# Kernel optimization log

Hardware: AMD Instinct MI355X
Metric: run time of the kernel (lower is better)

Reference implementation:

```python
import jax, jax.numpy as jnp
import numpy as np

ENCODER_DIM = 2048
DECODER_DIM = 512
ATTENTION_DIM = 512
BATCH = 512
NUM_PIXELS = 196


def setup_inputs() -> dict:
    key = jax.random.key(0)
    k = jax.random.split(key, 8)
    s_e = 1.0 / np.sqrt(ENCODER_DIM)
    s_d = 1.0 / np.sqrt(DECODER_DIM)
    s_a = 1.0 / np.sqrt(ATTENTION_DIM)
    return {
        "encoder_out": jax.random.normal(k[0], (BATCH, NUM_PIXELS, ENCODER_DIM), jnp.float32),
        "decoder_hidden": jax.random.normal(k[1], (BATCH, DECODER_DIM), jnp.float32),
        "W_enc": jax.random.uniform(k[2], (ENCODER_DIM, ATTENTION_DIM), jnp.float32, -s_e, s_e),
        "b_enc": jax.random.uniform(k[3], (ATTENTION_DIM,), jnp.float32, -s_e, s_e),
        "W_dec": jax.random.uniform(k[4], (DECODER_DIM, ATTENTION_DIM), jnp.float32, -s_d, s_d),
        "b_dec": jax.random.uniform(k[5], (ATTENTION_DIM,), jnp.float32, -s_d, s_d),
        "W_full": jax.random.uniform(k[6], (ATTENTION_DIM,), jnp.float32, -s_a, s_a),
        "b_full": jax.random.uniform(k[7], (), jnp.float32, -s_a, s_a),
    }


def reference(encoder_out, decoder_hidden, W_enc, b_enc, W_dec, b_dec, W_full, b_full):
    # att1: [B, P, A], att2: [B, A]
    att1 = jnp.einsum('bpe,ea->bpa', encoder_out, W_enc) + b_enc
    att2 = decoder_hidden @ W_dec + b_dec
    # scores: [B, P]
    scores = jnp.einsum('bpa,a->bp', jnp.tanh(att1 + att2[:, None, :]), W_full) + b_full
    alpha = jax.nn.softmax(scores, axis=1)
    context = jnp.einsum('bpe,bp->be', encoder_out, alpha)
    return context, alpha
```

## Files before the change

kernel.cpp:

```cpp
#include <hip/hip_runtime.h>
#include <hip/hip_bf16.h>
#include <stdint.h>

#define BATCH 512
#define PIX   196
#define EDIM  2048
#define DDIM  512
#define ADIM  512
#define MROWS (BATCH*PIX)

#define BM 256
#define BN 256
#define BK 64
#define NT (EDIM/BK)

typedef __attribute__((ext_vector_type(8))) short bf16x8;
typedef __attribute__((ext_vector_type(8))) float f32x8;
typedef __attribute__((ext_vector_type(8))) __bf16 bf16v8;
typedef __attribute__((ext_vector_type(4))) float f32x4;

#define GLL16(g, lptr) __builtin_amdgcn_global_load_lds( \
    (const __attribute__((address_space(1))) void*)(g),  \
    (__attribute__((address_space(3))) void*)(lptr), 16, 0, 0)

static __device__ __forceinline__ unsigned short f2bf(float f) {
  union { float f; uint32_t u; } v; v.f = f;
  uint32_t u = v.u;
  return (unsigned short)((u + 0x7FFFu + ((u >> 16) & 1u)) >> 16);
}

static __device__ __forceinline__ bf16x8 cvt8(float4 a, float4 b) {
  f32x8 v = {a.x, a.y, a.z, a.w, b.x, b.y, b.z, b.w};
  bf16v8 c = __builtin_convertvector(v, bf16v8);
  bf16x8 r;
  __builtin_memcpy(&r, &c, 16);
  return r;
}

__global__ void k_transpose_wenc(const float* __restrict__ W,
                                 unsigned short* __restrict__ Bt) {
  __shared__ float tile[32][33];
  const int kt = blockIdx.x;
  const int nt = blockIdx.y;
  const int tx = threadIdx.x, ty = threadIdx.y;
#pragma unroll
  for (int j = 0; j < 4; j++)
    tile[ty + 8*j][tx] = W[(size_t)(kt*32 + ty + 8*j)*ADIM + nt*32 + tx];
  __syncthreads();
#pragma unroll
  for (int j = 0; j < 4; j++)
    Bt[(size_t)(nt*32 + ty + 8*j)*EDIM + kt*32 + tx] = f2bf(tile[tx][ty + 8*j]);
}

__global__ void k_att2(const float* __restrict__ H, const float* __restrict__ Wd,
                       const float* __restrict__ bd, float* __restrict__ att2) {
  __shared__ float h[DDIM];
  const int b = blockIdx.x;
  const int t = threadIdx.x;
  h[t]       = H[(size_t)b*DDIM + t];
  h[t + 256] = H[(size_t)b*DDIM + t + 256];
  __syncthreads();
  float a0 = 0.f, a1 = 0.f;
#pragma unroll 8
  for (int k = 0; k < DDIM; k++) {
    const float hv = h[k];
    a0 += hv * Wd[(size_t)k*ADIM + t];
    a1 += hv * Wd[(size_t)k*ADIM + t + 256];
  }
  att2[(size_t)b*ADIM + t]       = a0 + bd[t];
  att2[(size_t)b*ADIM + t + 256] = a1 + bd[t + 256];
}

__global__ __launch_bounds__(512) void k_gemm_scores(
    const float* __restrict__ enc,
    const unsigned short* __restrict__ Bt,
    const float* __restrict__ b_enc,
    const float* __restrict__ att2,
    const float* __restrict__ W_full,
    float* __restrict__ scores)
{
  __shared__ __align__(16) char ldsA[2*32768];
  __shared__ __align__(16) char ldsB[2*32768];
  __shared__ float sc[BM];

  const int t   = threadIdx.x;
  const int l   = t & 63;
  const int wid = t >> 6;
  const int wr  = wid >> 2;
  const int wc  = wid & 3;

  const int orig = blockIdx.x;
  const int tile = (orig & 7) * 98 + (orig >> 3);
  const int bm0 = (tile >> 1) * BM;
  const int bn0 = (tile & 1) * BN;

  if (t < BM) sc[t] = 0.f;

  const int arow = t >> 1;
  const int ah   = t & 1;
  const float* srcA = enc + (size_t)(bm0 + arow) * EDIM + ah * 32;
  int wA[4];
#pragma unroll
  for (int j = 0; j < 4; j++)
    wA[j] = arow*128 + (((ah*4 + j) ^ (arow & 7)) * 16);

  const unsigned short* srcB[4];
#pragma unroll
  for (int j = 0; j < 4; j++) {
    const int row = (t >> 3) + j*64;
    srcB[j] = Bt + (size_t)(bn0 + row) * EDIM + ((t & 7) ^ (row & 7)) * 8;
  }
  const int dstB = wid * 1024;

  const int l15 = l & 15, hi = l >> 4;
  const int sw  = l15 & 7;
  const int c0  = (hi ^ sw) * 16;
  const int c1  = ((4 + hi) ^ sw) * 16;
  const int baseA = (wr*128 + l15) * 128;
  const int baseB = (wc*64  + l15) * 128;

  float4 ar[8];
  bf16x8 af[4], bfr[4];
  f32x4 acc[8][4] = {};

#define A_ISSUE(KT) do {                                         \
    const float* _s = srcA + (size_t)(KT) * BK;                  \
    _Pragma("unroll")                                            \
    for (int j = 0; j < 8; j++) ar[j] = ((const float4*)_s)[j];  \
  } while (0)

#define B_GLLJ(NXT, KT, J) \
    GLL16(srcB[J] + (size_t)(KT) * BK, ldsB + (NXT)*32768 + dstB + (J)*8192)

#define A_WRITE(NXT) do {                                        \
    _Pragma("unroll")                                            \
    for (int j = 0; j < 4; j++) {                                \
      bf16x8 w = cvt8(ar[2*j], ar[2*j + 1]);                     \
      *(bf16x8*)(ldsA + (NXT)*32768 + wA[j]) = w;                \
    }                                                            \
  } while (0)

#define DSREAD_B(CUR, CKS) do {                                  \
    _Pragma("unroll")                                            \
    for (int ni = 0; ni < 4; ni++)                               \
      bfr[ni] = *(const bf16x8*)(ldsB + (CUR)*32768 + baseB + ni*2048 + (CKS)); \
  } while (0)

#define DSREAD_A(CUR, CKS, MOFF) do {                            \
    _Pragma("unroll")                                            \
    for (int mi = 0; mi < 4; mi++)                               \
      af[mi] = *(const bf16x8*)(ldsA + (CUR)*32768 + baseA + (mi+(MOFF))*2048 + (CKS)); \
  } while (0)

#define BARLG()                                                  \
    __builtin_amdgcn_s_barrier();                                \
    asm volatile("s_waitcnt lgkmcnt(0)" ::: "memory");           \
    __builtin_amdgcn_sched_barrier(0);                           \
    __builtin_amdgcn_s_setprio(1)

#define ENDBAR()                                                 \
    __builtin_amdgcn_s_setprio(0);                               \
    __builtin_amdgcn_s_barrier()

#define MF16(MOFF) do {                                          \
    _Pragma("unroll")                                            \
    for (int mi = 0; mi < 4; mi++)                               \
      _Pragma("unroll")                                          \
      for (int ni = 0; ni < 4; ni++)                             \
        acc[mi+(MOFF)][ni] = __builtin_amdgcn_mfma_f32_16x16x32_bf16( \
            af[mi], bfr[ni], acc[mi+(MOFF)][ni], 0, 0, 0);       \
  } while (0)

#define TILE(KT, CUR, NXT) do {                                  \
                                                         \
    A_ISSUE((KT)+1);                                             \
    DSREAD_B(CUR, c0); DSREAD_A(CUR, c0, 0);                     \
    BARLG(); MF16(0); ENDBAR();                                  \
                                                         \
    B_GLLJ(NXT, (KT)+1, 0); B_GLLJ(NXT, (KT)+1, 1);              \
    DSREAD_A(CUR, c0, 4);                                        \
    BARLG(); MF16(4); ENDBAR();                                  \
                                                         \
    B_GLLJ(NXT, (KT)+1, 2); B_GLLJ(NXT, (KT)+1, 3);              \
    DSREAD_B(CUR, c1); DSREAD_A(CUR, c1, 0);                     \
    BARLG(); MF16(0); ENDBAR();                                  \
                                                         \
    asm volatile("s_waitcnt vmcnt(4)" ::: "memory");             \
    A_WRITE(NXT);                                                \
    DSREAD_A(CUR, c1, 4);                                        \
    BARLG(); MF16(4);                                            \
    asm volatile("s_waitcnt vmcnt(0)" ::: "memory");             \
    ENDBAR();                                                    \
  } while (0)

  A_ISSUE(0);
  B_GLLJ(0, 0, 0); B_GLLJ(0, 0, 1); B_GLLJ(0, 0, 2); B_GLLJ(0, 0, 3);
  asm volatile("s_waitcnt vmcnt(4)" ::: "memory");
  A_WRITE(0);
  asm volatile("s_waitcnt vmcnt(0) lgkmcnt(0)" ::: "memory");
  __builtin_amdgcn_s_barrier();

  for (int kb = 0; kb < 30; kb += 2) {
    TILE(kb,     0, 1);
    TILE(kb + 1, 1, 0);
  }
  TILE(30, 0, 1);

#pragma unroll
  for (int ks = 0; ks < 2; ks++) {
    const int cks = ks ? c1 : c0;
    DSREAD_B(1, cks);
    DSREAD_A(1, cks, 0);
    MF16(0);
    DSREAD_A(1, cks, 4);
    MF16(4);
  }

  float be[4], wf[4];
  int colv[4];
#pragma unroll
  for (int ni = 0; ni < 4; ni++) {
    colv[ni] = bn0 + wc*64 + ni*16 + l15;
    be[ni] = b_enc[colv[ni]];
    wf[ni] = W_full[colv[ni]];
  }
#pragma unroll
  for (int mi = 0; mi < 8; mi++) {
#pragma unroll
    for (int e = 0; e < 4; e++) {
      const int row_l = wr*128 + mi*16 + hi*4 + e;
      const unsigned gr = (unsigned)(bm0 + row_l);
      const unsigned b  = gr / 196u;
      float s = 0.f;
#pragma unroll
      for (int ni = 0; ni < 4; ni++) {
        const float v = acc[mi][ni][e] + be[ni] + att2[(size_t)b*ADIM + colv[ni]];
        s += tanhf(v) * wf[ni];
      }
      s += __shfl_xor(s, 1); s += __shfl_xor(s, 2);
      s += __shfl_xor(s, 4); s += __shfl_xor(s, 8);
      if (l15 == 0) atomicAdd(&sc[row_l], s);
    }
  }
  __syncthreads();
  if (t < BM) atomicAdd(&scores[bm0 + t], sc[t]);
}

__global__ void k_softmax(float* __restrict__ sa) {
  __shared__ float red[256];
  const int b = blockIdx.x, t = threadIdx.x;
  const float v = (t < PIX) ? sa[(size_t)b*PIX + t] : -1e30f;
  red[t] = v; __syncthreads();
  for (int s2 = 128; s2 > 0; s2 >>= 1) {
    if (t < s2) red[t] = fmaxf(red[t], red[t + s2]);
    __syncthreads();
  }
  const float m = red[0]; __syncthreads();
  const float e = (t < PIX) ? __expf(v - m) : 0.f;
  red[t] = e; __syncthreads();
  for (int s2 = 128; s2 > 0; s2 >>= 1) {
    if (t < s2) red[t] += red[t + s2];
    __syncthreads();
  }
  const float inv = 1.f / red[0];
  if (t < PIX) sa[(size_t)b*PIX + t] = e * inv;
}

__global__ __launch_bounds__(512) void k_context(
    const float* __restrict__ enc, const float* __restrict__ alpha,
    float* __restrict__ ctx) {
  __shared__ float al[PIX];
  const int b = blockIdx.x, t = threadIdx.x;
  if (t < PIX) al[t] = alpha[(size_t)b*PIX + t];
  __syncthreads();
  const float4* e4 = (const float4*)(enc + (size_t)b * PIX * EDIM);
  float4 acc = {0.f, 0.f, 0.f, 0.f};
#pragma unroll 4
  for (int p = 0; p < PIX; p++) {
    const float4 v = e4[(size_t)p * (EDIM/4) + t];
    const float a = al[p];
    acc.x += v.x * a; acc.y += v.y * a; acc.z += v.z * a; acc.w += v.w * a;
  }
  ((float4*)(ctx + (size_t)b * EDIM))[t] = acc;
}

extern "C" void kernel_launch(void* const* d_in, const int* in_sizes, int n_in,
                              void* d_out, int out_size, void* d_ws, size_t ws_size,
                              hipStream_t stream) {
  (void)in_sizes; (void)n_in; (void)out_size; (void)ws_size;
  const float* enc   = (const float*)d_in[0];
  const float* hid   = (const float*)d_in[1];
  const float* Wenc  = (const float*)d_in[2];
  const float* benc  = (const float*)d_in[3];
  const float* Wdec  = (const float*)d_in[4];
  const float* bdec  = (const float*)d_in[5];
  const float* Wfull = (const float*)d_in[6];

  unsigned short* Bt = (unsigned short*)d_ws;
  float* att2 = (float*)((char*)d_ws + (size_t)ADIM * EDIM * 2);
  float* ctx   = (float*)d_out;
  float* alpha = (float*)d_out + (size_t)BATCH * EDIM;

  hipMemsetAsync(alpha, 0, (size_t)MROWS * sizeof(float), stream);
  k_transpose_wenc<<<dim3(64, 16), dim3(32, 8), 0, stream>>>(Wenc, Bt);
  k_att2<<<BATCH, 256, 0, stream>>>(hid, Wdec, bdec, att2);
  k_gemm_scores<<<784, 512, 0, stream>>>(enc, Bt, benc, att2, Wfull, alpha);
  k_softmax<<<BATCH, 256, 0, stream>>>(alpha);
  k_context<<<BATCH, 512, 0, stream>>>(enc, alpha, ctx);
}
```

Before: 734.4 us.

## Stream fp32 A tiles directly to LDS with triple-buffered BK=32 pipeline

The fp32 encoder tile is now fetched with global_load_lds straight into LDS instead of through registers, and converted to bf16 when the MFMA fragments are read. The K-step shrinks from 64 to 32 and the loop uses three LDS buffers, prefetching two tiles ahead with partial vmcnt waits. This is meant to remove the register-staged load, convert and write path and deepen the load pipeline. In exchange, A LDS traffic doubles because it is stored as fp32, each wave repeats the fp32-to-bf16 conversion, and LDS use grows to about 144KB per block.

Result: faster. 667.3 us (-9.1%).

```diff
diff --git a/kernel.cpp b/kernel.cpp
--- a/kernel.cpp
+++ b/kernel.cpp
@@ -11,7 +11,7 @@
 
 #define BM 256
 #define BN 256
-#define BK 64
+#define BK 32
 #define NT (EDIM/BK)
 
 typedef __attribute__((ext_vector_type(8))) short bf16x8;
@@ -79,9 +79,10 @@
     const float* __restrict__ W_full,
     float* __restrict__ scores)
 {
-  __shared__ __align__(16) char ldsA[2*32768];
-  __shared__ __align__(16) char ldsB[2*32768];
+  __shared__ __align__(16) char ldsbuf[3*49152];
   __shared__ float sc[BM];
+  char* ldsA = ldsbuf;
+  char* ldsB = ldsbuf + 98304;
 
   const int t   = threadIdx.x;
   const int l   = t & 63;
@@ -96,60 +97,58 @@
 
   if (t < BM) sc[t] = 0.f;
 
-  const int arow = t >> 1;
-  const int ah   = t & 1;
-  const float* srcA = enc + (size_t)(bm0 + arow) * EDIM + ah * 32;
-  int wA[4];
-#pragma unroll
-  for (int j = 0; j < 4; j++)
-    wA[j] = arow*128 + (((ah*4 + j) ^ (arow & 7)) * 16);
-
-  const unsigned short* srcB[4];
+  const float* srcA[4];
 #pragma unroll
   for (int j = 0; j < 4; j++) {
-    const int row = (t >> 3) + j*64;
-    srcB[j] = Bt + (size_t)(bn0 + row) * EDIM + ((t & 7) ^ (row & 7)) * 8;
-  }
-  const int dstB = wid * 1024;
+    const int idx = j*512 + t;
+    const int row = idx >> 3, c = idx & 7;
+    srcA[j] = enc + (size_t)(bm0 + row) * EDIM + (c ^ (row & 7)) * 4;
+  }
+  const unsigned short* srcB[2];
+#pragma unroll
+  for (int j = 0; j < 2; j++) {
+    const int idx = j*512 + t;
+    const int row = idx >> 2, c = idx & 3;
+    srcB[j] = Bt + (size_t)(bn0 + row) * EDIM + (c ^ (row & 3)) * 8;
+  }
+  const int dstb = wid * 1024;
 
   const int l15 = l & 15, hi = l >> 4;
-  const int sw  = l15 & 7;
-  const int c0  = (hi ^ sw) * 16;
-  const int c1  = ((4 + hi) ^ sw) * 16;
-  const int baseA = (wr*128 + l15) * 128;
-  const int baseB = (wc*64  + l15) * 128;
-
-  float4 ar[8];
+  const int sw7 = l15 & 7, sw3 = l15 & 3;
+  const int addrA0 = (wr*128 + l15)*128 + (((2*hi)    ) ^ sw7)*16;
+  const int addrA1 = (wr*128 + l15)*128 + (((2*hi) + 1) ^ sw7)*16;
+  const int addrB  = (wc*64  + l15)*64  + (hi ^ sw3)*16;
+
   bf16x8 af[4], bfr[4];
   f32x4 acc[8][4] = {};
 
-#define A_ISSUE(KT) do {                                         \
-    const float* _s = srcA + (size_t)(KT) * BK;                  \
-    _Pragma("unroll")                                            \
-    for (int j = 0; j < 8; j++) ar[j] = ((const float4*)_s)[j];  \
-  } while (0)
-
-#define B_GLLJ(NXT, KT, J) \
-    GLL16(srcB[J] + (size_t)(KT) * BK, ldsB + (NXT)*32768 + dstB + (J)*8192)
-
-#define A_WRITE(NXT) do {                                        \
-    _Pragma("unroll")                                            \
-    for (int j = 0; j < 4; j++) {                                \
-      bf16x8 w = cvt8(ar[2*j], ar[2*j + 1]);                     \
-      *(bf16x8*)(ldsA + (NXT)*32768 + wA[j]) = w;                \
+#define A_GLL(WB, KT) do {                                       \
+    _Pragma("unroll")                                            \
+    for (int j = 0; j < 4; j++)                                  \
+      GLL16(srcA[j] + (size_t)(KT)*BK,                           \
+            ldsA + (WB)*32768 + j*8192 + dstb);                  \
+  } while (0)
+
+#define B_GLL(WB, KT) do {                                       \
+    _Pragma("unroll")                                            \
+    for (int j = 0; j < 2; j++)                                  \
+      GLL16(srcB[j] + (size_t)(KT)*BK,                           \
+            ldsB + (WB)*16384 + j*8192 + dstb);                  \
+  } while (0)
+
+#define DSREAD_A(BUF, MOFF) do {                                 \
+    _Pragma("unroll")                                            \
+    for (int mi = 0; mi < 4; mi++) {                             \
+      const float4 fa = *(const float4*)(ldsA + (BUF)*32768 + (mi+(MOFF))*2048 + addrA0); \
+      const float4 fb = *(const float4*)(ldsA + (BUF)*32768 + (mi+(MOFF))*2048 + addrA1); \
+      af[mi] = cvt8(fa, fb);                                     \
     }                                                            \
   } while (0)
 
-#define DSREAD_B(CUR, CKS) do {                                  \
+#define DSREAD_B(BUF) do {                                       \
     _Pragma("unroll")                                            \
     for (int ni = 0; ni < 4; ni++)                               \
-      bfr[ni] = *(const bf16x8*)(ldsB + (CUR)*32768 + baseB + ni*2048 + (CKS)); \
-  } while (0)
-
-#define DSREAD_A(CUR, CKS, MOFF) do {                            \
-    _Pragma("unroll")                                            \
-    for (int mi = 0; mi < 4; mi++)                               \
-      af[mi] = *(const bf16x8*)(ldsA + (CUR)*32768 + baseA + (mi+(MOFF))*2048 + (CKS)); \
+      bfr[ni] = *(const bf16x8*)(ldsB + (BUF)*16384 + ni*1024 + addrB); \
   } while (0)
 
 #define BARLG()                                                  \
@@ -171,50 +170,35 @@
             af[mi], bfr[ni], acc[mi+(MOFF)][ni], 0, 0, 0);       \
   } while (0)
 
-#define TILE(KT, CUR, NXT) do {                                  \
+#define TILE(T, BUF, WBUF, DO_STAGE, WVM) do {                   \
                                                          \
-    A_ISSUE((KT)+1);                                             \
-    DSREAD_B(CUR, c0); DSREAD_A(CUR, c0, 0);                     \
+    if (DO_STAGE) A_GLL(WBUF, (T)+2);                            \
+    DSREAD_B(BUF); DSREAD_A(BUF, 0);                             \
     BARLG(); MF16(0); ENDBAR();                                  \
                                                          \
-    B_GLLJ(NXT, (KT)+1, 0); B_GLLJ(NXT, (KT)+1, 1);              \
-    DSREAD_A(CUR, c0, 4);                                        \
-    BARLG(); MF16(4); ENDBAR();                                  \
-                                                         \
-    B_GLLJ(NXT, (KT)+1, 2); B_GLLJ(NXT, (KT)+1, 3);              \
-    DSREAD_B(CUR, c1); DSREAD_A(CUR, c1, 0);                     \
-    BARLG(); MF16(0); ENDBAR();                                  \
-                                                         \
-    asm volatile("s_waitcnt vmcnt(4)" ::: "memory");             \
-    A_WRITE(NXT);                                                \
-    DSREAD_A(CUR, c1, 4);                                        \
+    if (DO_STAGE) B_GLL(WBUF, (T)+2);                            \
+    DSREAD_A(BUF, 4);                                            \
     BARLG(); MF16(4);                                            \
-    asm volatile("s_waitcnt vmcnt(0)" ::: "memory");             \
+    if ((WVM) == 6)      asm volatile("s_waitcnt vmcnt(6)" ::: "memory"); \
+    else if ((WVM) == 0) asm volatile("s_waitcnt vmcnt(0)" ::: "memory"); \
     ENDBAR();                                                    \
   } while (0)
 
-  A_ISSUE(0);
-  B_GLLJ(0, 0, 0); B_GLLJ(0, 0, 1); B_GLLJ(0, 0, 2); B_GLLJ(0, 0, 3);
-  asm volatile("s_waitcnt vmcnt(4)" ::: "memory");
-  A_WRITE(0);
-  asm volatile("s_waitcnt vmcnt(0) lgkmcnt(0)" ::: "memory");
+  A_GLL(0, 0); B_GLL(0, 0);
+  A_GLL(1, 1); B_GLL(1, 1);
+  asm volatile("s_waitcnt vmcnt(6)" ::: "memory");
   __builtin_amdgcn_s_barrier();
 
-  for (int kb = 0; kb < 30; kb += 2) {
-    TILE(kb,     0, 1);
-    TILE(kb + 1, 1, 0);
-  }
-  TILE(30, 0, 1);
-
-#pragma unroll
-  for (int ks = 0; ks < 2; ks++) {
-    const int cks = ks ? c1 : c0;
-    DSREAD_B(1, cks);
-    DSREAD_A(1, cks, 0);
-    MF16(0);
-    DSREAD_A(1, cks, 4);
-    MF16(4);
-  }
+  for (int kb = 0; kb < 60; kb += 3) {
+    TILE(kb,     0, 2, true, 6);
+    TILE(kb + 1, 1, 0, true, 6);
+    TILE(kb + 2, 2, 1, true, 6);
+  }
+  TILE(60, 0, 2, true, 6);
+  TILE(61, 1, 0, true, 6);
+  TILE(62, 2, 2, false, 0);
+  DSREAD_B(0); DSREAD_A(0, 0); MF16(0);
+  DSREAD_A(0, 4); MF16(4);
 
   float be[4], wf[4];
   int colv[4];
```
